# Kernel tuning notes

Measured on AMD Instinct MI355X. Metric: run time of the kernel, lower is better.

The kernel has to match this reference:

```python
import jax, jax.numpy as jnp
import numpy as np

BS, S, DM, H, DK, FF = 4, 512, 1024, 16, 64, 4096


def _ln(x, g, b, eps=1e-5):
    m = jnp.mean(x, -1, keepdims=True)
    v = jnp.mean((x - m) ** 2, -1, keepdims=True)
    return (x - m) / jnp.sqrt(v + eps) * g + b


def setup_inputs() -> dict:
    key = jax.random.key(0)
    ks = jax.random.split(key, 10)
    w = lambda k, shape: jax.random.normal(k, shape, jnp.float32) * 0.02
    return dict(
        x=jax.random.normal(ks[0], (BS, S, DM), jnp.float32),
        eos_mask=jnp.ones((BS, 1, S, S), bool),
        prior=jnp.zeros((1,), jnp.float32),
        gn_g=jnp.ones((DM,), jnp.float32), gn_b=jnp.zeros((DM,), jnp.float32),
        wq=w(ks[1], (DK, DK)), bq=jnp.zeros((DK,), jnp.float32),
        wk=w(ks[2], (DK, DK)), bk=jnp.zeros((DK,), jnp.float32),
        fq_w=w(ks[3], (DM, DM)), fq_b=jnp.zeros((DM,), jnp.float32),
        fk_w=w(ks[4], (DM, DM)), fk_b=jnp.zeros((DM,), jnp.float32),
        fv_w=w(ks[5], (DM, DM)), fv_b=jnp.zeros((DM,), jnp.float32),
        ln1_g=jnp.ones((DM,), jnp.float32), ln1_b=jnp.zeros((DM,), jnp.float32),
        ff_w1=w(ks[6], (DM, FF)), ff_b1=jnp.zeros((FF,), jnp.float32),
        ff_w2=w(ks[7], (FF, DM)), ff_b2=jnp.zeros((DM,), jnp.float32),
        ln2_g=jnp.ones((DM,), jnp.float32), ln2_b=jnp.zeros((DM,), jnp.float32),
    )


def reference(x, eos_mask, prior, gn_g, gn_b, wq, bq, wk, bk,
              fq_w, fq_b, fk_w, fk_b, fv_w, fv_b,
              ln1_g, ln1_b, ff_w1, ff_b1, ff_w2, ff_b2, ln2_g, ln2_b):
    bs, s, dm = x.shape
    eye = jnp.eye(s, dtype=jnp.float32)                      # b diag
    offdiag = jnp.eye(s, k=1, dtype=jnp.float32) + jnp.eye(s, k=-1, dtype=jnp.float32)  # a + c
    tri = jnp.triu(jnp.ones((s, s), jnp.float32))            # upper-tri incl diag

    # ---- GroupAttention ----
    ctx = _ln(x, gn_g, gn_b).reshape(bs, s, H, DK).transpose(0, 2, 1, 3)  # b h s d
    q = ctx @ wq + bq
    k = ctx @ wk + bk
    scores = jnp.einsum('bhqd,bhkd->bhqk', q, k) / DK
    m = jnp.logical_and(eos_mask, offdiag > 0)
    scores = jnp.where(m, scores, -10000.0)
    na = jax.nn.softmax(scores, axis=-1)
    na = jnp.sqrt(na * jnp.swapaxes(na, -1, -2) + 1e-4)
    na = prior + (1.0 - prior) * na
    t = jnp.where(offdiag == 0, 0.0, jnp.log(na + 1e-9)) @ tri  # b h s s
    g = jnp.exp(tri @ t)
    g = jnp.where((tri - eye) == 0, 0.0, g)
    group_prob = g + jnp.swapaxes(g, -1, -2) + jnp.where(eye == 0, 1e-4, na)

    # ---- self-attention sublayer (pre-norm residual) ----
    # NOTE: the original torch code's attention_mask masked_fill is non-inplace
    # and its result is discarded, so the mask has NO effect here (faithful).
    xn = _ln(x, ln1_g, ln1_b)
    q2 = (xn @ fq_w + fq_b).reshape(bs, s, H, DK).transpose(0, 2, 1, 3)
    k2 = (xn @ fk_w + fk_b).reshape(bs, s, H, DK).transpose(0, 2, 1, 3)
    v2 = (xn @ fv_w + fv_b).reshape(bs, s, H, DK).transpose(0, 2, 1, 3)
    att = jnp.einsum('bhqd,bhkd->bhqk', q2, k2) / np.float32(np.sqrt(DK))
    att = jax.nn.softmax(att, axis=-1) * group_prob
    sa = jnp.einsum('bhqk,bhkd->bhqd', att, v2).transpose(0, 2, 1, 3).reshape(bs, s, dm)
    x = x + sa

    # ---- FFN sublayer ----
    xn2 = _ln(x, ln2_g, ln2_b)
    ff = jax.nn.relu(xn2 @ ff_w1 + ff_b1) @ ff_w2 + ff_b2
    x = x + ff
    return (x, group_prob, na)
```

## Files before the change

kernel.cpp:

```cpp
#include <hip/hip_runtime.h>
#include <hip/hip_bf16.h>


#define BS   4
#define S    512
#define DM   1024
#define H    16
#define DK   64
#define FF   4096

typedef unsigned short u16;
typedef __attribute__((ext_vector_type(8))) short bf16x8;
typedef __attribute__((ext_vector_type(4))) float f32x4;

static constexpr size_t XSZ   = (size_t)BS * S * DM;
static constexpr size_t ATTSZ = (size_t)BS * H * S * S;

__device__ __forceinline__ u16 f2bf(float f) {
    union { float f; unsigned u; } v; v.f = f;
    unsigned u = v.u;
    return (u16)((u + 0x7FFFu + ((u >> 16) & 1u)) >> 16);
}
__device__ __forceinline__ float bf2f(u16 h) {
    union { unsigned u; float f; } v; v.u = ((unsigned)h) << 16;
    return v.f;
}

__device__ __forceinline__ void gload16(const void* g, void* lds) {
    __builtin_amdgcn_global_load_lds(
        (const __attribute__((address_space(1))) unsigned int*)g,
        (__attribute__((address_space(3))) unsigned int*)lds,
        16, 0, 0);
}

template <int NF>
__device__ __forceinline__ void mfma_loop(
    const u16* __restrict__ Ag,
    const u16* __restrict__ Bg,
    int lda, int ldb, int K,
    u16* As, u16* Bs,
    f32x4 (&acc)[4][NF])
{
    const int tid  = threadIdx.x;
    const int lane = tid & 63;
    const int wv   = tid >> 6;
    const int wr   = wv >> 1, wc = wv & 1;
    const int arow = lane & 15;
    const int ak   = (lane >> 4) * 8;
    constexpr int BROWS = 2 * NF * 16;
    constexpr int BISS  = BROWS / 64;

    for (int k0 = 0; k0 < K; k0 += 32) {
#pragma unroll
        for (int i = 0; i < 2; ++i) {
            int chunk = i * 256 + tid;
            int r = chunk >> 2, c = chunk & 3;
            gload16(Ag + (size_t)r * lda + k0 + c * 8,
                    &As[(i * 256 + wv * 64) * 8]);
        }
#pragma unroll
        for (int i = 0; i < BISS; ++i) {
            int chunk = i * 256 + tid;
            int r = chunk >> 2, c = chunk & 3;
            gload16(Bg + (size_t)r * ldb + k0 + c * 8,
                    &Bs[(i * 256 + wv * 64) * 8]);
        }
        __syncthreads();
        bf16x8 af[4], bfr[NF];
#pragma unroll
        for (int mi = 0; mi < 4; ++mi)
            af[mi] = *(const bf16x8*)&As[(wr * 64 + mi * 16 + arow) * 32 + ak];
#pragma unroll
        for (int nj = 0; nj < NF; ++nj)
            bfr[nj] = *(const bf16x8*)&Bs[(wc * NF * 16 + nj * 16 + arow) * 32 + ak];
#pragma unroll
        for (int mi = 0; mi < 4; ++mi)
#pragma unroll
            for (int nj = 0; nj < NF; ++nj)
                acc[mi][nj] = __builtin_amdgcn_mfma_f32_16x16x32_bf16(
                    af[mi], bfr[nj], acc[mi][nj], 0, 0, 0);
        __syncthreads();
    }
}

__global__ __launch_bounds__(256) void transcvt(
    const float* __restrict__ src, u16* __restrict__ dst, int K, int N)
{
    __shared__ __align__(16) u16 T[64][80];
    int k0 = blockIdx.x * 64, n0 = blockIdx.y * 64, tid = threadIdx.x;
    int r = tid >> 2, c0 = (tid & 3) * 16;
#pragma unroll
    for (int i = 0; i < 4; ++i) {
        float4 v = *(const float4*)&src[(size_t)(k0 + r) * N + n0 + c0 + i * 4];
        T[c0 + i * 4 + 0][r] = f2bf(v.x);
        T[c0 + i * 4 + 1][r] = f2bf(v.y);
        T[c0 + i * 4 + 2][r] = f2bf(v.z);
        T[c0 + i * 4 + 3][r] = f2bf(v.w);
    }
    __syncthreads();
    int n = tid >> 2, kc = (tid & 3) * 16;
#pragma unroll
    for (int i = 0; i < 2; ++i) {
        ushort4 a = *(const ushort4*)&T[n][kc + i * 8];
        ushort4 b = *(const ushort4*)&T[n][kc + i * 8 + 4];
        *(ushort4*)&dst[(size_t)(n0 + n) * K + k0 + kc + i * 8]     = a;
        *(ushort4*)&dst[(size_t)(n0 + n) * K + k0 + kc + i * 8 + 4] = b;
    }
}

__global__ __launch_bounds__(256) void ln_dual_kernel(
    const float* __restrict__ x,
    const float* __restrict__ g1, const float* __restrict__ b1,
    const float* __restrict__ g2, const float* __restrict__ b2,
    float* __restrict__ o1, u16* __restrict__ o2)
{
    __shared__ float sred[8];
    int row = blockIdx.x, tid = threadIdx.x;
    const float4 v = ((const float4*)(x + (size_t)row * DM))[tid];
    float s = v.x + v.y + v.z + v.w;
    float q = v.x * v.x + v.y * v.y + v.z * v.z + v.w * v.w;
#pragma unroll
    for (int o = 32; o > 0; o >>= 1) { s += __shfl_down(s, o); q += __shfl_down(q, o); }
    if ((tid & 63) == 0) { sred[(tid >> 6) * 2] = s; sred[(tid >> 6) * 2 + 1] = q; }
    __syncthreads();
    s = sred[0] + sred[2] + sred[4] + sred[6];
    q = sred[1] + sred[3] + sred[5] + sred[7];
    float mean = s * (1.f / DM);
    float var  = q * (1.f / DM) - mean * mean;
    float rstd = rsqrtf(var + 1e-5f);
    float4 G1 = ((const float4*)g1)[tid], B1 = ((const float4*)b1)[tid];
    float4 G2 = ((const float4*)g2)[tid], B2 = ((const float4*)b2)[tid];
    float n0 = (v.x - mean) * rstd, n1 = (v.y - mean) * rstd;
    float n2 = (v.z - mean) * rstd, n3 = (v.w - mean) * rstd;
    float4 r1;
    r1.x = n0 * G1.x + B1.x; r1.y = n1 * G1.y + B1.y;
    r1.z = n2 * G1.z + B1.z; r1.w = n3 * G1.w + B1.w;
    ((float4*)(o1 + (size_t)row * DM))[tid] = r1;
    ushort4 r2;
    r2.x = f2bf(n0 * G2.x + B2.x); r2.y = f2bf(n1 * G2.y + B2.y);
    r2.z = f2bf(n2 * G2.z + B2.z); r2.w = f2bf(n3 * G2.w + B2.w);
    ((ushort4*)(o2 + (size_t)row * DM))[tid] = r2;
}

__global__ __launch_bounds__(256) void ln_bf16_kernel(
    const float* __restrict__ x,
    const float* __restrict__ g1, const float* __restrict__ b1,
    u16* __restrict__ o1)
{
    __shared__ float sred[8];
    int row = blockIdx.x, tid = threadIdx.x;
    const float4 v = ((const float4*)(x + (size_t)row * DM))[tid];
    float s = v.x + v.y + v.z + v.w;
    float q = v.x * v.x + v.y * v.y + v.z * v.z + v.w * v.w;
#pragma unroll
    for (int o = 32; o > 0; o >>= 1) { s += __shfl_down(s, o); q += __shfl_down(q, o); }
    if ((tid & 63) == 0) { sred[(tid >> 6) * 2] = s; sred[(tid >> 6) * 2 + 1] = q; }
    __syncthreads();
    s = sred[0] + sred[2] + sred[4] + sred[6];
    q = sred[1] + sred[3] + sred[5] + sred[7];
    float mean = s * (1.f / DM);
    float var  = q * (1.f / DM) - mean * mean;
    float rstd = rsqrtf(var + 1e-5f);
    float4 G1 = ((const float4*)g1)[tid], B1 = ((const float4*)b1)[tid];
    ushort4 r1;
    r1.x = f2bf((v.x - mean) * rstd * G1.x + B1.x);
    r1.y = f2bf((v.y - mean) * rstd * G1.y + B1.y);
    r1.z = f2bf((v.z - mean) * rstd * G1.z + B1.z);
    r1.w = f2bf((v.w - mean) * rstd * G1.w + B1.w);
    ((ushort4*)(o1 + (size_t)row * DM))[tid] = r1;
}

__global__ __launch_bounds__(512) void groupqk_kernel(
    const float* __restrict__ ctx,
    const float* __restrict__ wq, const float* __restrict__ bq,
    const float* __restrict__ wk, const float* __restrict__ bk,
    float* __restrict__ qg, float* __restrict__ kg)
{
    __shared__ float Wq[64][65], Wk[64][65], Ct[8][65];
    int tid = threadIdx.x;
    for (int t = tid; t < 4096; t += 512) {
        Wq[t >> 6][t & 63] = wq[t];
        Wk[t >> 6][t & 63] = wk[t];
    }
    int blk = blockIdx.x;
    int bh = blk >> 6;
    int i0 = (blk & 63) * 8;
    int b = bh >> 4, h = bh & 15;
    {
        int r = tid >> 6, c = tid & 63;
        Ct[r][c] = ctx[((size_t)b * S + i0 + r) * DM + h * 64 + c];
    }
    __syncthreads();
    int r = tid >> 6, j = tid & 63;
    float aq = bq[j], ak = bk[j];
#pragma unroll
    for (int d = 0; d < 64; ++d) {
        float c = Ct[r][d];
        aq = fmaf(c, Wq[d][j], aq);
        ak = fmaf(c, Wk[d][j], ak);
    }
    size_t o = ((size_t)bh * S + i0 + r) * DK + j;
    qg[o] = aq;
    kg[o] = ak;
}

__global__ __launch_bounds__(256) void adj_kernel(
    const float* __restrict__ qg, const float* __restrict__ kg,
    const int* __restrict__ eos, const float* __restrict__ prior,
    float* __restrict__ nap, float* __restrict__ Pout)
{
    __shared__ float su[S], sl[S], nu[S], nl[S], cl[S];
    int tid = threadIdx.x, bh = blockIdx.x, b = bh >> 4;
    const float* qb = qg + (size_t)bh * S * DK;
    const float* kb = kg + (size_t)bh * S * DK;
    for (int i = tid; i < S; i += 256) {
        float du = 0.f, dl = 0.f;
        const float* qi = qb + (size_t)i * DK;
        if (i < S - 1) {
            const float* kn = kb + (size_t)(i + 1) * DK;
            for (int d = 0; d < DK; ++d) du = fmaf(qi[d], kn[d], du);
        }
        if (i > 0) {
            const float* kp = kb + (size_t)(i - 1) * DK;
            for (int d = 0; d < DK; ++d) dl = fmaf(qi[d], kp[d], dl);
        }
        su[i] = du * (1.f / DK);
        sl[i] = dl * (1.f / DK);
    }
    __syncthreads();
    for (int i = tid; i < S; i += 256) {
        bool vu = (i < S - 1) && (eos[(size_t)b * S * S + (size_t)i * S + (i + 1)] != 0);
        bool vl = (i > 0)     && (eos[(size_t)b * S * S + (size_t)i * S + (i - 1)] != 0);
        float eu = 0.f, el = 0.f;
        if (vu && vl) {
            float m = fmaxf(su[i], sl[i]);
            eu = expf(su[i] - m);
            el = expf(sl[i] - m);
        } else if (vu) eu = 1.f;
        else if (vl) el = 1.f;
        float Z = eu + el;
        if (Z == 0.f) Z = 1.f;
        nu[i] = eu / Z;
        nl[i] = el / Z;
    }
    __syncthreads();
    float pr = prior[0];
    for (int i = tid; i < S - 1; i += 256) {
        float v = sqrtf(nu[i] * nl[i + 1] + 1e-4f);
        v = pr + (1.f - pr) * v;
        nap[(size_t)bh * S + i] = v;
        cl[i] = logf(v + 1e-9f);
    }
    if (tid == 0) cl[S - 1] = 0.f;
    __syncthreads();
    if (tid < 64) {
        float loc[8];
        float s8 = 0.f;
#pragma unroll
        for (int e = 0; e < 8; ++e) { loc[e] = cl[tid * 8 + e]; s8 += loc[e]; }
        float v = s8;
#pragma unroll
        for (int o = 1; o < 64; o <<= 1) {
            float n = __shfl_up(v, o);
            if (tid >= o) v += n;
        }
        float run = v - s8;
        float* Pb = Pout + (size_t)bh * S;
#pragma unroll
        for (int e = 0; e < 8; ++e) { Pb[tid * 8 + e] = run; run += loc[e]; }
    }
}

__global__ void na_fill_kernel(const float* __restrict__ nap,
                               const float* __restrict__ prior,
                               float* __restrict__ out_na)
{
    float pr = prior[0];
    float base = pr + (1.f - pr) * 0.01f;
    size_t n4 = ATTSZ / 4;
    for (size_t t = (size_t)blockIdx.x * 256 + threadIdx.x; t < n4;
         t += (size_t)gridDim.x * 256) {
        size_t e = t * 4;
        int bh = (int)(e >> 18);
        int rem = (int)(e & 262143);
        int i = rem >> 9;
        int j0 = rem & 511;
        float4 v;
        float* vp = &v.x;
#pragma unroll
        for (int jj = 0; jj < 4; ++jj) {
            int j = j0 + jj;
            float val = base;
            if (j == i + 1)      val = nap[(size_t)bh * S + i];
            else if (j + 1 == i) val = nap[(size_t)bh * S + j];
            vp[jj] = val;
        }
        ((float4*)out_na)[t] = v;
    }
}

__global__ __launch_bounds__(256) void gp_fill_kernel(
    const float* __restrict__ Pin, const float* __restrict__ prior,
    float* __restrict__ out_gp)
{
    __shared__ float Pl[S];
    int bh = blockIdx.y;
    int i0 = blockIdx.x * 4;
    int tid = threadIdx.x;
    Pl[tid]       = Pin[(size_t)bh * S + tid];
    Pl[tid + 256] = Pin[(size_t)bh * S + tid + 256];
    __syncthreads();
    float pr = prior[0];
    float base = pr + (1.f - pr) * 0.01f;
    int r  = tid >> 6;
    int j0 = (tid & 63) * 8;
    int i  = i0 + r;
    float vals[8];
#pragma unroll
    for (int jj = 0; jj < 8; ++jj) {
        int j = j0 + jj;
        float val;
        if (i == j) {
            val = base;
        } else {
            int a = min(i, j), bb = max(i, j);
            float t1 = Pl[min(bb, S - 2) + 1] - Pl[max(a - 1, 0)];
            float t2 = Pl[min(bb - 1, S - 2) + 1] - Pl[a];
            val = expf(t1 + t2) + 1e-4f;
        }
        vals[jj] = val;
    }
    float* orow = out_gp + ((size_t)bh * S + i) * S + j0;
    *(float4*)&orow[0] = *(float4*)&vals[0];
    *(float4*)&orow[4] = *(float4*)&vals[4];
}

__global__ __launch_bounds__(256) void qkv_gemm(
    const u16* __restrict__ xn, const u16* __restrict__ wqkvT,
    const float* __restrict__ bq_, const float* __restrict__ bk_,
    const float* __restrict__ bv_,
    u16* __restrict__ q2, u16* __restrict__ k2, u16* __restrict__ v2T)
{
    __shared__ __align__(16) u16 As[128 * 32], Bs[128 * 32];
    int m0 = blockIdx.y * 128, n0 = blockIdx.x * 128;
    f32x4 acc[4][4] = {};
    mfma_loop<4>(xn + (size_t)m0 * DM, wqkvT + (size_t)n0 * DM, DM, DM, DM,
                 As, Bs, acc);
    int tid = threadIdx.x, lane = tid & 63, wv = tid >> 6;
    int wr = wv >> 1, wc = wv & 1;
    int region = n0 >> 10;
    const float* bias = region == 0 ? bq_ : (region == 1 ? bk_ : bv_);
    int b = m0 >> 9;
    if (region < 2) {
        u16* dst = region == 0 ? q2 : k2;
#pragma unroll
        for (int mi = 0; mi < 4; ++mi) {
#pragma unroll
            for (int nj = 0; nj < 4; ++nj) {
                int nn = (n0 + wc * 64 + nj * 16 + (lane & 15)) & 1023;
                int h = nn >> 6, d = nn & 63;
                float bv = bias[nn];
#pragma unroll
                for (int reg = 0; reg < 4; ++reg) {
                    int s = (m0 & 511) + wr * 64 + mi * 16 + (lane >> 4) * 4 + reg;
                    dst[((size_t)(b * H + h) * S + s) * DK + d] =
                        f2bf(acc[mi][nj][reg] + bv);
                }
            }
        }
    } else {
#pragma unroll
        for (int mi = 0; mi < 4; ++mi) {
            int s0 = (m0 & 511) + wr * 64 + mi * 16 + (lane >> 4) * 4;
#pragma unroll
            for (int nj = 0; nj < 4; ++nj) {
                int nn = (n0 + wc * 64 + nj * 16 + (lane & 15)) & 1023;
                int h = nn >> 6, d = nn & 63;
                float bv = bias[nn];
                ushort4 pk;
                pk.x = f2bf(acc[mi][nj][0] + bv);
                pk.y = f2bf(acc[mi][nj][1] + bv);
                pk.z = f2bf(acc[mi][nj][2] + bv);
                pk.w = f2bf(acc[mi][nj][3] + bv);
                *(ushort4*)&v2T[((size_t)(b * H + h) * DK + d) * S + s0] = pk;
            }
        }
    }
}

__global__ __launch_bounds__(256) void ffn1_gemm(
    const u16* __restrict__ xn2, const u16* __restrict__ w1T,
    const float* __restrict__ b1, u16* __restrict__ h1)
{
    __shared__ __align__(16) u16 As[128 * 32], Bs[128 * 32];
    int m0 = blockIdx.y * 128, n0 = blockIdx.x * 128;
    f32x4 acc[4][4] = {};
    mfma_loop<4>(xn2 + (size_t)m0 * DM, w1T + (size_t)n0 * DM, DM, DM, DM,
                 As, Bs, acc);
    int tid = threadIdx.x, lane = tid & 63, wv = tid >> 6;
    int wr = wv >> 1, wc = wv & 1;
#pragma unroll
    for (int mi = 0; mi < 4; ++mi) {
#pragma unroll
        for (int nj = 0; nj < 4; ++nj) {
            int n = n0 + wc * 64 + nj * 16 + (lane & 15);
            float bv = b1[n];
#pragma unroll
            for (int reg = 0; reg < 4; ++reg) {
                int m = m0 + wr * 64 + mi * 16 + (lane >> 4) * 4 + reg;
                h1[(size_t)m * FF + n] = f2bf(fmaxf(acc[mi][nj][reg] + bv, 0.f));
            }
        }
    }
}

__global__ __launch_bounds__(256) void ffn2_gemm(
    const u16* __restrict__ h1, const u16* __restrict__ w2T,
    const float* __restrict__ b2, const float* __restrict__ xmid,
    float* __restrict__ out_x)
{
    __shared__ __align__(16) u16 As[128 * 32], Bs[64 * 32];
    int m0 = blockIdx.y * 128, n0 = blockIdx.x * 64;
    f32x4 acc[4][2] = {};
    mfma_loop<2>(h1 + (size_t)m0 * FF, w2T + (size_t)n0 * FF, FF, FF, FF,
                 As, Bs, acc);
    int tid = threadIdx.x, lane = tid & 63, wv = tid >> 6;
    int wr = wv >> 1, wc = wv & 1;
#pragma unroll
    for (int mi = 0; mi < 4; ++mi) {
#pragma unroll
        for (int nj = 0; nj < 2; ++nj) {
            int n = n0 + wc * 32 + nj * 16 + (lane & 15);
            float bv = b2[n];
#pragma unroll
            for (int reg = 0; reg < 4; ++reg) {
                int m = m0 + wr * 64 + mi * 16 + (lane >> 4) * 4 + reg;
                size_t o = (size_t)m * DM + n;
                out_x[o] = acc[mi][nj][reg] + bv + xmid[o];
            }
        }
    }
}

__global__ __launch_bounds__(256) void scores_gemm(
    const u16* __restrict__ q2, const u16* __restrict__ k2,
    u16* __restrict__ att)
{
    __shared__ __align__(16) u16 As[128 * 32], Bs[128 * 32];
    int bh = blockIdx.z;
    int m0 = blockIdx.y * 128, n0 = blockIdx.x * 128;
    f32x4 acc[4][4] = {};
    mfma_loop<4>(q2 + ((size_t)bh * S + m0) * DK,
                 k2 + ((size_t)bh * S + n0) * DK, DK, DK, DK, As, Bs, acc);
    int tid = threadIdx.x, lane = tid & 63, wv = tid >> 6;
    int wr = wv >> 1, wc = wv & 1;
    u16* C = att + (size_t)bh * S * S;
#pragma unroll
    for (int mi = 0; mi < 4; ++mi) {
#pragma unroll
        for (int nj = 0; nj < 4; ++nj) {
            int n = n0 + wc * 64 + nj * 16 + (lane & 15);
#pragma unroll
            for (int reg = 0; reg < 4; ++reg) {
                int m = m0 + wr * 64 + mi * 16 + (lane >> 4) * 4 + reg;
                C[(size_t)m * S + n] = f2bf(acc[mi][nj][reg] * 0.125f);
            }
        }
    }
}

__global__ __launch_bounds__(256) void softmax_gp_kernel(
    u16* __restrict__ att, const float* __restrict__ gp)
{
    __shared__ float sred[4];
    size_t row = blockIdx.x;
    u16* ar = att + row * S;
    const float* gr = gp + row * S;
    int tid = threadIdx.x;
    ushort2 v = ((const ushort2*)ar)[tid];
    float a0 = bf2f(v.x), a1 = bf2f(v.y);
    float m = fmaxf(a0, a1);
#pragma unroll
    for (int o = 32; o > 0; o >>= 1) m = fmaxf(m, __shfl_down(m, o));
    if ((tid & 63) == 0) sred[tid >> 6] = m;
    __syncthreads();
    m = fmaxf(fmaxf(sred[0], sred[1]), fmaxf(sred[2], sred[3]));
    float e0 = expf(a0 - m), e1 = expf(a1 - m);
    float s = e0 + e1;
#pragma unroll
    for (int o = 32; o > 0; o >>= 1) s += __shfl_down(s, o);
    __syncthreads();
    if ((tid & 63) == 0) sred[tid >> 6] = s;
    __syncthreads();
    s = sred[0] + sred[1] + sred[2] + sred[3];
    float inv = 1.f / s;
    float2 g = ((const float2*)gr)[tid];
    ushort2 o2;
    o2.x = f2bf(e0 * inv * g.x);
    o2.y = f2bf(e1 * inv * g.y);
    ((ushort2*)ar)[tid] = o2;
}

__global__ __launch_bounds__(256) void pv_gemm(
    const u16* __restrict__ att, const u16* __restrict__ v2T,
    const float* __restrict__ x, float* __restrict__ xmid)
{
    __shared__ __align__(16) u16 As[128 * 32], Bs[64 * 32];
    int bh = blockIdx.z, b = bh >> 4, h = bh & 15;
    int m0 = blockIdx.y * 128;
    f32x4 acc[4][2] = {};
    mfma_loop<2>(att + ((size_t)bh * S + m0) * S,
                 v2T + (size_t)bh * DK * S, S, S, S, As, Bs, acc);
    int tid = threadIdx.x, lane = tid & 63, wv = tid >> 6;
    int wr = wv >> 1, wc = wv & 1;
#pragma unroll
    for (int mi = 0; mi < 4; ++mi) {
#pragma unroll
        for (int nj = 0; nj < 2; ++nj) {
            int d = wc * 32 + nj * 16 + (lane & 15);
#pragma unroll
            for (int reg = 0; reg < 4; ++reg) {
                int s = m0 + wr * 64 + mi * 16 + (lane >> 4) * 4 + reg;
                size_t o = ((size_t)b * S + s) * DM + h * 64 + d;
                xmid[o] = x[o] + acc[mi][nj][reg];
            }
        }
    }
}

extern "C" void kernel_launch(void* const* d_in, const int* in_sizes, int n_in,
                              void* d_out, int out_size, void* d_ws, size_t ws_size,
                              hipStream_t stream)
{
    const float* x     = (const float*)d_in[0];
    const int*   eos   = (const int*)d_in[1];
    const float* prior = (const float*)d_in[2];
    const float* gn_g  = (const float*)d_in[3];
    const float* gn_b  = (const float*)d_in[4];
    const float* wq    = (const float*)d_in[5];
    const float* bq    = (const float*)d_in[6];
    const float* wk    = (const float*)d_in[7];
    const float* bk    = (const float*)d_in[8];
    const float* fq_w  = (const float*)d_in[9];
    const float* fq_b  = (const float*)d_in[10];
    const float* fk_w  = (const float*)d_in[11];
    const float* fk_b  = (const float*)d_in[12];
    const float* fv_w  = (const float*)d_in[13];
    const float* fv_b  = (const float*)d_in[14];
    const float* ln1_g = (const float*)d_in[15];
    const float* ln1_b = (const float*)d_in[16];
    const float* ff_w1 = (const float*)d_in[17];
    const float* ff_b1 = (const float*)d_in[18];
    const float* ff_w2 = (const float*)d_in[19];
    const float* ff_b2 = (const float*)d_in[20];
    const float* ln2_g = (const float*)d_in[21];
    const float* ln2_b = (const float*)d_in[22];

    char* W = (char*)d_ws;
    float* ctx   = (float*)(W + 0);
    u16*   q2    = (u16*)(W + 0);
    u16*   k2    = (u16*)(W + ((size_t)4 << 20));
    u16*   xn    = (u16*)(W + ((size_t)8 << 20));
    float* qg    = (float*)(W + ((size_t)12 << 20));
    float* xmid  = (float*)(W + ((size_t)12 << 20));
    float* kg    = (float*)(W + ((size_t)20 << 20));
    u16*   v2T   = (u16*)(W + ((size_t)20 << 20));
    u16*   xn2   = (u16*)(W + ((size_t)24 << 20));
    float* nap   = (float*)(W + ((size_t)28 << 20));
    float* Pp    = (float*)(W + ((size_t)28 << 20) + (128 << 10));
    u16*   att   = (u16*)(W + ((size_t)29 << 20));
    u16*   h1    = (u16*)(W + ((size_t)29 << 20));
    u16*   wqkvT = (u16*)(W + ((size_t)61 << 20));
    u16*   w1T   = (u16*)(W + ((size_t)67 << 20));
    u16*   w2T   = (u16*)(W + ((size_t)75 << 20));

    float* out_x  = (float*)d_out;
    float* out_gp = out_x + XSZ;
    float* out_na = out_gp + ATTSZ;

    const int NTOK = BS * S;

    transcvt<<<dim3(16, 16), 256, 0, stream>>>(fq_w, wqkvT, DM, DM);
    transcvt<<<dim3(16, 16), 256, 0, stream>>>(fk_w, wqkvT + (size_t)DM * DM, DM, DM);
    transcvt<<<dim3(16, 16), 256, 0, stream>>>(fv_w, wqkvT + 2 * (size_t)DM * DM, DM, DM);
    transcvt<<<dim3(16, 64), 256, 0, stream>>>(ff_w1, w1T, DM, FF);
    transcvt<<<dim3(64, 16), 256, 0, stream>>>(ff_w2, w2T, FF, DM);
    ln_dual_kernel<<<NTOK, 256, 0, stream>>>(x, gn_g, gn_b, ln1_g, ln1_b, ctx, xn);
    groupqk_kernel<<<BS * H * (S / 8), 512, 0, stream>>>(ctx, wq, bq, wk, bk, qg, kg);
    adj_kernel<<<BS * H, 256, 0, stream>>>(qg, kg, eos, prior, nap, Pp);
    na_fill_kernel<<<2048, 256, 0, stream>>>(nap, prior, out_na);
    gp_fill_kernel<<<dim3(S / 4, BS * H), 256, 0, stream>>>(Pp, prior, out_gp);
    qkv_gemm<<<dim3(24, 16), 256, 0, stream>>>(xn, wqkvT, fq_b, fk_b, fv_b,
                                               q2, k2, v2T);
    scores_gemm<<<dim3(4, 4, BS * H), 256, 0, stream>>>(q2, k2, att);
    softmax_gp_kernel<<<BS * H * S, 256, 0, stream>>>(att, out_gp);
    pv_gemm<<<dim3(1, 4, BS * H), 256, 0, stream>>>(att, v2T, x, xmid);
    ln_bf16_kernel<<<NTOK, 256, 0, stream>>>(xmid, ln2_g, ln2_b, xn2);
    ffn1_gemm<<<dim3(32, 16), 256, 0, stream>>>(xn2, w1T, ff_b1, h1);
    ffn2_gemm<<<dim3(16, 16), 256, 0, stream>>>(h1, w2T, ff_b2, xmid, out_x);
}
```

Measured before the change: 470.5 us.

## Double-buffer GEMM tiles, merge weight transposes, fuse output fills, warp-per-row softmax

The shared MFMA loop now double-buffers its LDS tiles, so the global-to-LDS loads for the next K-slice are issued before the current slice is computed. LDS allocations in all GEMM kernels are doubled to hold both buffers. The five weight transpose/convert launches become one grid-indexed kernel, and the na and group_prob fills become one kernel. Softmax now uses one wavefront per row with shuffle-only reductions and no max subtraction, which removes block syncs but depends on scores staying small enough not to overflow exp.

```diff
diff --git a/kernel.cpp b/kernel.cpp
--- a/kernel.cpp
+++ b/kernel.cpp
@@ -34,9 +34,48 @@
 }
 
 template <int NF>
+__device__ __forceinline__ void stage32(
+    const u16* __restrict__ Ag, const u16* __restrict__ Bg,
+    int lda, int ldb, int k0, u16* As, u16* Bs, int tid, int wv)
+{
+#pragma unroll
+    for (int i = 0; i < 2; ++i) {
+        int chunk = i * 256 + tid;
+        int r = chunk >> 2, c = chunk & 3;
+        gload16(Ag + (size_t)r * lda + k0 + c * 8, &As[(i * 256 + wv * 64) * 8]);
+    }
+    constexpr int BISS = (2 * NF * 16) / 64;
+#pragma unroll
+    for (int i = 0; i < BISS; ++i) {
+        int chunk = i * 256 + tid;
+        int r = chunk >> 2, c = chunk & 3;
+        gload16(Bg + (size_t)r * ldb + k0 + c * 8, &Bs[(i * 256 + wv * 64) * 8]);
+    }
+}
+
+template <int NF>
+__device__ __forceinline__ void compute32(
+    const u16* As, const u16* Bs, f32x4 (&acc)[4][NF],
+    int wr, int wc, int arow, int ak)
+{
+    bf16x8 af[4], bfr[NF];
+#pragma unroll
+    for (int mi = 0; mi < 4; ++mi)
+        af[mi] = *(const bf16x8*)&As[(wr * 64 + mi * 16 + arow) * 32 + ak];
+#pragma unroll
+    for (int nj = 0; nj < NF; ++nj)
+        bfr[nj] = *(const bf16x8*)&Bs[(wc * NF * 16 + nj * 16 + arow) * 32 + ak];
+#pragma unroll
+    for (int mi = 0; mi < 4; ++mi)
+#pragma unroll
+        for (int nj = 0; nj < NF; ++nj)
+            acc[mi][nj] = __builtin_amdgcn_mfma_f32_16x16x32_bf16(
+                af[mi], bfr[nj], acc[mi][nj], 0, 0, 0);
+}
+
+template <int NF>
 __device__ __forceinline__ void mfma_loop(
-    const u16* __restrict__ Ag,
-    const u16* __restrict__ Bg,
+    const u16* __restrict__ Ag, const u16* __restrict__ Bg,
     int lda, int ldb, int K,
     u16* As, u16* Bs,
     f32x4 (&acc)[4][NF])
@@ -48,46 +87,47 @@
     const int arow = lane & 15;
     const int ak   = (lane >> 4) * 8;
     constexpr int BROWS = 2 * NF * 16;
-    constexpr int BISS  = BROWS / 64;
-
-    for (int k0 = 0; k0 < K; k0 += 32) {
-#pragma unroll
-        for (int i = 0; i < 2; ++i) {
-            int chunk = i * 256 + tid;
-            int r = chunk >> 2, c = chunk & 3;
-            gload16(Ag + (size_t)r * lda + k0 + c * 8,
-                    &As[(i * 256 + wv * 64) * 8]);
-        }
-#pragma unroll
-        for (int i = 0; i < BISS; ++i) {
-            int chunk = i * 256 + tid;
-            int r = chunk >> 2, c = chunk & 3;
-            gload16(Bg + (size_t)r * ldb + k0 + c * 8,
-                    &Bs[(i * 256 + wv * 64) * 8]);
-        }
+    u16* As0 = As;             u16* As1 = As + 128 * 32;
+    u16* Bs0 = Bs;             u16* Bs1 = Bs + BROWS * 32;
+    const int nt = K >> 5;
+
+    stage32<NF>(Ag, Bg, lda, ldb, 0, As0, Bs0, tid, wv);
+    __syncthreads();
+    for (int t = 0; t < nt; t += 2) {
+        stage32<NF>(Ag, Bg, lda, ldb, (t + 1) << 5, As1, Bs1, tid, wv);
+        compute32<NF>(As0, Bs0, acc, wr, wc, arow, ak);
         __syncthreads();
-        bf16x8 af[4], bfr[NF];
-#pragma unroll
-        for (int mi = 0; mi < 4; ++mi)
-            af[mi] = *(const bf16x8*)&As[(wr * 64 + mi * 16 + arow) * 32 + ak];
-#pragma unroll
-        for (int nj = 0; nj < NF; ++nj)
-            bfr[nj] = *(const bf16x8*)&Bs[(wc * NF * 16 + nj * 16 + arow) * 32 + ak];
-#pragma unroll
-        for (int mi = 0; mi < 4; ++mi)
-#pragma unroll
-            for (int nj = 0; nj < NF; ++nj)
-                acc[mi][nj] = __builtin_amdgcn_mfma_f32_16x16x32_bf16(
-                    af[mi], bfr[nj], acc[mi][nj], 0, 0, 0);
+        if (t + 2 < nt)
+            stage32<NF>(Ag, Bg, lda, ldb, (t + 2) << 5, As0, Bs0, tid, wv);
+        compute32<NF>(As1, Bs1, acc, wr, wc, arow, ak);
         __syncthreads();
     }
 }
 
-__global__ __launch_bounds__(256) void transcvt(
-    const float* __restrict__ src, u16* __restrict__ dst, int K, int N)
+__global__ __launch_bounds__(256) void transcvt_all(
+    const float* __restrict__ fq_w, const float* __restrict__ fk_w,
+    const float* __restrict__ fv_w, const float* __restrict__ ff_w1,
+    const float* __restrict__ ff_w2,
+    u16* __restrict__ wqkvT, u16* __restrict__ w1T, u16* __restrict__ w2T)
 {
     __shared__ __align__(16) u16 T[64][80];
-    int k0 = blockIdx.x * 64, n0 = blockIdx.y * 64, tid = threadIdx.x;
+    int blk = blockIdx.x, tid = threadIdx.x;
+    const float* src; u16* dst; int K, N, kb, nb;
+    if (blk < 768) {
+        int w = blk >> 8, rem = blk & 255;
+        src = w == 0 ? fq_w : (w == 1 ? fk_w : fv_w);
+        dst = wqkvT + (size_t)w * DM * DM;
+        K = DM; N = DM; kb = rem & 15; nb = rem >> 4;
+    } else if (blk < 1792) {
+        int rem = blk - 768;
+        src = ff_w1; dst = w1T; K = DM; N = FF;
+        kb = rem & 15; nb = rem >> 4;
+    } else {
+        int rem = blk - 1792;
+        src = ff_w2; dst = w2T; K = FF; N = DM;
+        kb = rem & 63; nb = rem >> 6;
+    }
+    int k0 = kb * 64, n0 = nb * 64;
     int r = tid >> 2, c0 = (tid & 3) * 16;
 #pragma unroll
     for (int i = 0; i < 4; ++i) {
@@ -271,37 +311,10 @@
     }
 }
 
-__global__ void na_fill_kernel(const float* __restrict__ nap,
-                               const float* __restrict__ prior,
-                               float* __restrict__ out_na)
-{
-    float pr = prior[0];
-    float base = pr + (1.f - pr) * 0.01f;
-    size_t n4 = ATTSZ / 4;
-    for (size_t t = (size_t)blockIdx.x * 256 + threadIdx.x; t < n4;
-         t += (size_t)gridDim.x * 256) {
-        size_t e = t * 4;
-        int bh = (int)(e >> 18);
-        int rem = (int)(e & 262143);
-        int i = rem >> 9;
-        int j0 = rem & 511;
-        float4 v;
-        float* vp = &v.x;
-#pragma unroll
-        for (int jj = 0; jj < 4; ++jj) {
-            int j = j0 + jj;
-            float val = base;
-            if (j == i + 1)      val = nap[(size_t)bh * S + i];
-            else if (j + 1 == i) val = nap[(size_t)bh * S + j];
-            vp[jj] = val;
-        }
-        ((float4*)out_na)[t] = v;
-    }
-}
-
-__global__ __launch_bounds__(256) void gp_fill_kernel(
-    const float* __restrict__ Pin, const float* __restrict__ prior,
-    float* __restrict__ out_gp)
+__global__ __launch_bounds__(256) void fill_gp_na_kernel(
+    const float* __restrict__ Pin, const float* __restrict__ nap,
+    const float* __restrict__ prior,
+    float* __restrict__ out_gp, float* __restrict__ out_na)
 {
     __shared__ float Pl[S];
     int bh = blockIdx.y;
@@ -315,7 +328,9 @@
     int r  = tid >> 6;
     int j0 = (tid & 63) * 8;
     int i  = i0 + r;
-    float vals[8];
+    float na_i   = (i < S - 1) ? nap[(size_t)bh * S + i]     : base;
+    float na_im1 = (i > 0)     ? nap[(size_t)bh * S + i - 1] : base;
+    float vals[8], nvals[8];
 #pragma unroll
     for (int jj = 0; jj < 8; ++jj) {
         int j = j0 + jj;
@@ -329,10 +344,17 @@
             val = expf(t1 + t2) + 1e-4f;
         }
         vals[jj] = val;
+        float nv = base;
+        if (j == i + 1)      nv = na_i;
+        else if (j + 1 == i) nv = na_im1;
+        nvals[jj] = nv;
     }
     float* orow = out_gp + ((size_t)bh * S + i) * S + j0;
     *(float4*)&orow[0] = *(float4*)&vals[0];
     *(float4*)&orow[4] = *(float4*)&vals[4];
+    float* nrow = out_na + ((size_t)bh * S + i) * S + j0;
+    *(float4*)&nrow[0] = *(float4*)&nvals[0];
+    *(float4*)&nrow[4] = *(float4*)&nvals[4];
 }
 
 __global__ __launch_bounds__(256) void qkv_gemm(
@@ -341,7 +363,7 @@
     const float* __restrict__ bv_,
     u16* __restrict__ q2, u16* __restrict__ k2, u16* __restrict__ v2T)
 {
-    __shared__ __align__(16) u16 As[128 * 32], Bs[128 * 32];
+    __shared__ __align__(16) u16 As[2 * 128 * 32], Bs[2 * 128 * 32];
     int m0 = blockIdx.y * 128, n0 = blockIdx.x * 128;
     f32x4 acc[4][4] = {};
     mfma_loop<4>(xn + (size_t)m0 * DM, wqkvT + (size_t)n0 * DM, DM, DM, DM,
@@ -392,7 +414,7 @@
     const u16* __restrict__ xn2, const u16* __restrict__ w1T,
     const float* __restrict__ b1, u16* __restrict__ h1)
 {
-    __shared__ __align__(16) u16 As[128 * 32], Bs[128 * 32];
+    __shared__ __align__(16) u16 As[2 * 128 * 32], Bs[2 * 128 * 32];
     int m0 = blockIdx.y * 128, n0 = blockIdx.x * 128;
     f32x4 acc[4][4] = {};
     mfma_loop<4>(xn2 + (size_t)m0 * DM, w1T + (size_t)n0 * DM, DM, DM, DM,
@@ -419,7 +441,7 @@
     const float* __restrict__ b2, const float* __restrict__ xmid,
     float* __restrict__ out_x)
 {
-    __shared__ __align__(16) u16 As[128 * 32], Bs[64 * 32];
+    __shared__ __align__(16) u16 As[2 * 128 * 32], Bs[2 * 64 * 32];
     int m0 = blockIdx.y * 128, n0 = blockIdx.x * 64;
     f32x4 acc[4][2] = {};
     mfma_loop<2>(h1 + (size_t)m0 * FF, w2T + (size_t)n0 * FF, FF, FF, FF,
@@ -446,7 +468,7 @@
     const u16* __restrict__ q2, const u16* __restrict__ k2,
     u16* __restrict__ att)
 {
-    __shared__ __align__(16) u16 As[128 * 32], Bs[128 * 32];
+    __shared__ __align__(16) u16 As[2 * 128 * 32], Bs[2 * 128 * 32];
     int bh = blockIdx.z;
     int m0 = blockIdx.y * 128, n0 = blockIdx.x * 128;
     f32x4 acc[4][4] = {};
@@ -472,40 +494,37 @@
 __global__ __launch_bounds__(256) void softmax_gp_kernel(
     u16* __restrict__ att, const float* __restrict__ gp)
 {
-    __shared__ float sred[4];
-    size_t row = blockIdx.x;
+    size_t row = (size_t)blockIdx.x * 4 + (threadIdx.x >> 6);
+    int lane = threadIdx.x & 63;
     u16* ar = att + row * S;
     const float* gr = gp + row * S;
-    int tid = threadIdx.x;
-    ushort2 v = ((const ushort2*)ar)[tid];
-    float a0 = bf2f(v.x), a1 = bf2f(v.y);
-    float m = fmaxf(a0, a1);
-#pragma unroll
-    for (int o = 32; o > 0; o >>= 1) m = fmaxf(m, __shfl_down(m, o));
-    if ((tid & 63) == 0) sred[tid >> 6] = m;
-    __syncthreads();
-    m = fmaxf(fmaxf(sred[0], sred[1]), fmaxf(sred[2], sred[3]));
-    float e0 = expf(a0 - m), e1 = expf(a1 - m);
-    float s = e0 + e1;
-#pragma unroll
-    for (int o = 32; o > 0; o >>= 1) s += __shfl_down(s, o);
-    __syncthreads();
-    if ((tid & 63) == 0) sred[tid >> 6] = s;
-    __syncthreads();
-    s = sred[0] + sred[1] + sred[2] + sred[3];
+    bf16x8 v = *(const bf16x8*)&ar[lane * 8];
+    float e[8];
+    float s = 0.f;
+#pragma unroll
+    for (int j = 0; j < 8; ++j) { e[j] = expf(bf2f((u16)v[j])); s += e[j]; }
+#pragma unroll
+    for (int o = 1; o < 64; o <<= 1) s += __shfl_xor(s, o);
     float inv = 1.f / s;
-    float2 g = ((const float2*)gr)[tid];
-    ushort2 o2;
-    o2.x = f2bf(e0 * inv * g.x);
-    o2.y = f2bf(e1 * inv * g.y);
-    ((ushort2*)ar)[tid] = o2;
+    float4 g0 = *(const float4*)&gr[lane * 8];
+    float4 g1 = *(const float4*)&gr[lane * 8 + 4];
+    bf16x8 o8;
+    o8[0] = (short)f2bf(e[0] * inv * g0.x);
+    o8[1] = (short)f2bf(e[1] * inv * g0.y);
+    o8[2] = (short)f2bf(e[2] * inv * g0.z);
+    o8[3] = (short)f2bf(e[3] * inv * g0.w);
+    o8[4] = (short)f2bf(e[4] * inv * g1.x);
+    o8[5] = (short)f2bf(e[5] * inv * g1.y);
+    o8[6] = (short)f2bf(e[6] * inv * g1.z);
+    o8[7] = (short)f2bf(e[7] * inv * g1.w);
+    *(bf16x8*)&ar[lane * 8] = o8;
 }
 
 __global__ __launch_bounds__(256) void pv_gemm(
     const u16* __restrict__ att, const u16* __restrict__ v2T,
     const float* __restrict__ x, float* __restrict__ xmid)
 {
-    __shared__ __align__(16) u16 As[128 * 32], Bs[64 * 32];
+    __shared__ __align__(16) u16 As[2 * 128 * 32], Bs[2 * 64 * 32];
     int bh = blockIdx.z, b = bh >> 4, h = bh & 15;
     int m0 = blockIdx.y * 128;
     f32x4 acc[4][2] = {};
@@ -580,20 +599,17 @@
 
     const int NTOK = BS * S;
 
-    transcvt<<<dim3(16, 16), 256, 0, stream>>>(fq_w, wqkvT, DM, DM);
-    transcvt<<<dim3(16, 16), 256, 0, stream>>>(fk_w, wqkvT + (size_t)DM * DM, DM, DM);
-    transcvt<<<dim3(16, 16), 256, 0, stream>>>(fv_w, wqkvT + 2 * (size_t)DM * DM, DM, DM);
-    transcvt<<<dim3(16, 64), 256, 0, stream>>>(ff_w1, w1T, DM, FF);
-    transcvt<<<dim3(64, 16), 256, 0, stream>>>(ff_w2, w2T, FF, DM);
+    transcvt_all<<<2816, 256, 0, stream>>>(fq_w, fk_w, fv_w, ff_w1, ff_w2,
+                                           wqkvT, w1T, w2T);
     ln_dual_kernel<<<NTOK, 256, 0, stream>>>(x, gn_g, gn_b, ln1_g, ln1_b, ctx, xn);
     groupqk_kernel<<<BS * H * (S / 8), 512, 0, stream>>>(ctx, wq, bq, wk, bk, qg, kg);
     adj_kernel<<<BS * H, 256, 0, stream>>>(qg, kg, eos, prior, nap, Pp);
-    na_fill_kernel<<<2048, 256, 0, stream>>>(nap, prior, out_na);
-    gp_fill_kernel<<<dim3(S / 4, BS * H), 256, 0, stream>>>(Pp, prior, out_gp);
+    fill_gp_na_kernel<<<dim3(S / 4, BS * H), 256, 0, stream>>>(
+        Pp, nap, prior, out_gp, out_na);
     qkv_gemm<<<dim3(24, 16), 256, 0, stream>>>(xn, wqkvT, fq_b, fk_b, fv_b,
                                                q2, k2, v2T);
     scores_gemm<<<dim3(4, 4, BS * H), 256, 0, stream>>>(q2, k2, att);
-    softmax_gp_kernel<<<BS * H * S, 256, 0, stream>>>(att, out_gp);
+    softmax_gp_kernel<<<BS * H * S / 4, 256, 0, stream>>>(att, out_gp);
     pv_gemm<<<dim3(1, 4, BS * H), 256, 0, stream>>>(att, v2T, x, xmid);
     ln_bf16_kernel<<<NTOK, 256, 0, stream>>>(xmid, ln2_g, ln2_b, xn2);
     ffn1_gemm<<<dim3(32, 16), 256, 0, stream>>>(xn2, w1T, ff_b1, h1);
```

New measurement: 463.2 us. No clear change (-1.5%).
